# Optimization experiments

Hardware: AMD Instinct MI355X
Metric: run time of the kernel (lower is better)

Reference implementation:

```python
import jax, jax.numpy as jnp
import numpy as np
import math

B, S, DIM, H = 2, 2048, 1024, 16
DH = DIM // H          # 64, per-head dim
DFF = 2048             # FCLayer hidden
NEG = -1.0e9


def setup_inputs() -> dict:
    key = jax.random.key(0)
    ks = jax.random.split(key, 10)
    glorot = jax.nn.initializers.glorot_uniform()
    de_x = jax.random.normal(ks[0], (B, S, DIM), dtype=jnp.float32)
    en_x = jax.random.normal(ks[1], (B, S, DIM), dtype=jnp.float32)
    # causal mask: 1.0 where attention is disallowed (upper triangle)
    mask = jnp.triu(jnp.ones((S, S), dtype=jnp.float32), k=1)
    # Stacked per-head projection weights for the (shared) attn_heads.
    Wq = glorot(ks[2], (H, DIM, DH), jnp.float32)
    Wk = glorot(ks[3], (H, DIM, DH), jnp.float32)
    Wv = glorot(ks[4], (H, DIM, DH), jnp.float32)
    W1 = glorot(ks[5], (DIM, DFF), jnp.float32)
    b1 = jnp.zeros((DFF,), jnp.float32)
    W2 = glorot(ks[6], (DFF, DIM), jnp.float32)
    b2 = jnp.zeros((DIM,), jnp.float32)
    return {"de_x": de_x, "en_x": en_x, "mask": mask,
            "Wq": Wq, "Wk": Wk, "Wv": Wv,
            "W1": W1, "b1": b1, "W2": W2, "b2": b2}


def _multihead(q_x, k_x, v_x, Wq, Wk, Wv, mask):
    # q_x/k_x/v_x: [B,S,DIM]; W*: [H,DIM,DH]
    q = jnp.einsum('bsd,hde->bhse', q_x, Wq)
    k = jnp.einsum('bsd,hde->bhse', k_x, Wk)
    v = jnp.einsum('bsd,hde->bhse', v_x, Wv)
    p = jnp.einsum('bhse,bhte->bhst', q, k) / math.sqrt(DH)
    if mask is not None:
        p = p + mask * NEG
    p = jax.nn.softmax(p, axis=-1)
    h = jnp.einsum('bhst,bhte->bhse', p, v)      # [B,H,S,DH]
    # concat heads along feature dim -> [B,S,DIM]
    return h.transpose(0, 2, 1, 3).reshape(q_x.shape[0], q_x.shape[1], -1)


def reference(de_x, en_x, mask, Wq, Wk, Wv, W1, b1, W2, b2):
    # Faithful to the source: compute_multihead_output ignores its attn_heads
    # arg and always uses self.attn_heads, and binds head(q=outer_en, k=outer_en,
    # v=outer_de). So:
    #   h1 = MHA(q=de_x, k=de_x, v=de_x, mask) with attn_heads weights
    #   h2 = MHA(q=en_x, k=en_x, v=h1, None)   with the SAME weights
    h1 = _multihead(de_x, de_x, de_x, Wq, Wk, Wv, mask)
    h2 = _multihead(en_x, en_x, h1, Wq, Wk, Wv, None)
    ff1 = jax.nn.relu(h2 @ W1 + b1)
    y = ff1 @ W2 + b2
    return y
```

## Files before the change

kernel.cpp:

```cpp
#include <hip/hip_runtime.h>
#include <stdint.h>


#define DEV static __device__ __forceinline__

typedef __attribute__((ext_vector_type(8))) __bf16 bf16x8;
typedef __attribute__((ext_vector_type(8))) unsigned short u16x8;
typedef __attribute__((ext_vector_type(2))) uint32_t u32x2;
typedef __attribute__((ext_vector_type(4))) float f32x4;

DEV float bf2f(uint16_t u) { union { uint32_t u; float f; } v; v.u = ((uint32_t)u) << 16; return v.f; }
DEV uint16_t f2bf(float f) {
  union { float f; uint32_t u; } v; v.f = f;
  uint32_t r = v.u + 0x7fffu + ((v.u >> 16) & 1u);
  return (uint16_t)(r >> 16);
}
DEV uint16_t f2bf_hw(float f) { return __builtin_bit_cast(unsigned short, (__bf16)f); }

DEV bf16x8 asbf(u16x8 v) { return __builtin_bit_cast(bf16x8, v); }
DEV f32x4 mfma32(bf16x8 a, bf16x8 b, f32x4 c) {
  return __builtin_amdgcn_mfma_f32_16x16x32_bf16(a, b, c, 0, 0, 0);
}

DEV void gload_lds16(const void* g, void* l) {
  __builtin_amdgcn_global_load_lds(
      (const __attribute__((address_space(1))) uint32_t*)g,
      (__attribute__((address_space(3))) uint32_t*)l, 16, 0, 0);
}

DEV int swz(int row, int slot) { return slot ^ (row & 7); }

DEV bf16x8 frag8(const uint16_t* l, int row, int slot) {
  u16x8 v = *(const u16x8*)((const char*)l + row * 128 + (swz(row, slot) << 4));
  return asbf(v);
}

__global__ void probe_k(const uint32_t* __restrict__ mask, uint32_t* __restrict__ flag) {
  flag[0] = (mask[1] & 0xFFFFu) ? 1u : 0u;
}

__global__ __launch_bounds__(256) void cvt_k(const void* __restrict__ src,
                                             uint16_t* __restrict__ dst, int n,
                                             const uint32_t* __restrict__ flag) {
  if (flag[0]) return;
  const int stride = gridDim.x * 256 * 8;
  for (int i = (blockIdx.x * 256 + threadIdx.x) * 8; i < n; i += stride) {
    const float* sf = (const float*)src + i;
    u16x8 o;
    for (int j = 0; j < 8; j++) o[j] = f2bf(sf[j]);
    *(u16x8*)(dst + i) = o;
  }
}

__global__ __launch_bounds__(256) void transpose_k(const void* __restrict__ in_,
                                                   uint16_t* __restrict__ out, int R, int C,
                                                   float scale,
                                                   const uint32_t* __restrict__ flag) {
  __shared__ uint16_t t[32][33];
  const int isbf = (int)flag[0];
  const int b = blockIdx.z;
  const float* in_f = (const float*)in_ + (size_t)b * R * C;
  const uint16_t* in_u = (const uint16_t*)in_ + (size_t)b * R * C;
  out += (size_t)b * R * C;
  const int c0 = blockIdx.x * 32, r0 = blockIdx.y * 32;
  const int tx = threadIdx.x & 31, ty = threadIdx.x >> 5;
  for (int i = 0; i < 4; i++) {
    int r = ty + i * 8;
    size_t idx = (size_t)(r0 + r) * C + c0 + tx;
    uint16_t v;
    if (isbf) v = (scale == 1.0f) ? in_u[idx] : f2bf(bf2f(in_u[idx]) * scale);
    else      v = f2bf(in_f[idx] * scale);
    t[r][tx] = v;
  }
  __syncthreads();
  for (int i = 0; i < 4; i++) {
    int r = ty + i * 8;
    out[(size_t)(c0 + r) * R + r0 + tx] = t[tx][r];
  }
}

__global__ __launch_bounds__(256) void transpose_qkv_k(const void* __restrict__ Wq,
                                                       const void* __restrict__ Wk,
                                                       const void* __restrict__ Wv,
                                                       uint16_t* __restrict__ out,
                                                       const uint32_t* __restrict__ flag) {
  __shared__ uint16_t t[32][33];
  const int isbf = (int)flag[0];
  const int which = blockIdx.z >> 4, hh = blockIdx.z & 15;
  const void* in_ = (which == 0 ? Wq : which == 1 ? Wk : Wv);
  const float scale = (which == 0) ? 0.180336880f : 1.0f;
  const int R = 1024, C = 64;
  const float* in_f = (const float*)in_ + (size_t)hh * R * C;
  const uint16_t* in_u = (const uint16_t*)in_ + (size_t)hh * R * C;
  out += ((size_t)which * 16 + hh) * R * C;
  const int c0 = blockIdx.x * 32, r0 = blockIdx.y * 32;
  const int tx = threadIdx.x & 31, ty = threadIdx.x >> 5;
  for (int i = 0; i < 4; i++) {
    int r = ty + i * 8;
    size_t idx = (size_t)(r0 + r) * C + c0 + tx;
    uint16_t v;
    if (isbf) v = (scale == 1.0f) ? in_u[idx] : f2bf(bf2f(in_u[idx]) * scale);
    else      v = f2bf(in_f[idx] * scale);
    t[r][tx] = v;
  }
  __syncthreads();
  for (int i = 0; i < 4; i++) {
    int r = ty + i * 8;
    out[(size_t)(c0 + r) * R + r0 + tx] = t[tx][r];
  }
}

__global__ __launch_bounds__(256) void proj_k(
    const uint16_t* __restrict__ Aqk_c, const void* __restrict__ Aqk_r,
    const uint16_t* __restrict__ Av_c, const void* __restrict__ Av_r,
    const uint16_t* __restrict__ Wt,
    uint16_t* __restrict__ Q, uint16_t* __restrict__ K, uint16_t* __restrict__ Vt,
    const uint32_t* __restrict__ flag) {
  __shared__ __attribute__((aligned(16))) uint16_t lA[2][128 * 64];
  __shared__ __attribute__((aligned(16))) uint16_t lB[2][128 * 64];
  const int isbf = (int)flag[0];
  const uint16_t* Aqk = isbf ? (const uint16_t*)Aqk_r : Aqk_c;
  const uint16_t* Av  = isbf ? (const uint16_t*)Av_r  : Av_c;
  const int tid = threadIdx.x, lane = tid & 63, wave = tid >> 6;
  const int g = lane >> 4;
  const int m0 = blockIdx.x * 128, n0 = blockIdx.y * 128;
  const int proj = n0 >> 10;
  const uint16_t* A = (proj == 2 ? Av : Aqk);
  const uint16_t* Bt = Wt + (size_t)n0 * 1024;
  const int wm = wave >> 1, wn = wave & 1;
  f32x4 acc[4][4] = {};
  u16x8 ra[4], rb[4];
  const int row0 = tid >> 3, slot0 = tid & 7;
  auto loadT = [&](int kt) {
    for (int i = 0; i < 4; i++) {
      int row = row0 + i * 32;
      ra[i] = *(const u16x8*)(A + (size_t)(m0 + row) * 1024 + kt + slot0 * 8);
      rb[i] = *(const u16x8*)(Bt + (size_t)row * 1024 + kt + slot0 * 8);
    }
  };
  auto writeT = [&](int buf) {
    for (int i = 0; i < 4; i++) {
      int row = row0 + i * 32;
      *(u16x8*)&lA[buf][(row * 8 + swz(row, slot0)) * 8] = ra[i];
      *(u16x8*)&lB[buf][(row * 8 + swz(row, slot0)) * 8] = rb[i];
    }
  };
  loadT(0);
  writeT(0);
  int cur = 0;
  for (int it = 0; it < 16; it++) {
    const int more = (it < 15);
    if (more) loadT((it + 1) * 64);
    __syncthreads();
    for (int kk = 0; kk < 2; kk++) {
      bf16x8 af[4], bfr[4];
      for (int fm = 0; fm < 4; fm++) af[fm] = frag8(lA[cur], wm * 64 + fm * 16 + (lane & 15), kk * 4 + g);
      for (int fn = 0; fn < 4; fn++) bfr[fn] = frag8(lB[cur], wn * 64 + fn * 16 + (lane & 15), kk * 4 + g);
      for (int fm = 0; fm < 4; fm++)
        for (int fn = 0; fn < 4; fn++)
          acc[fm][fn] = mfma32(af[fm], bfr[fn], acc[fm][fn]);
    }
    if (more) writeT(cur ^ 1);
    cur ^= 1;
  }
  if (proj != 2) {
    uint16_t* outp = (proj == 0 ? Q : K);
    for (int fm = 0; fm < 4; fm++)
      for (int fn = 0; fn < 4; fn++)
        for (int r = 0; r < 4; r++) {
          int row = m0 + wm * 64 + fm * 16 + g * 4 + r;
          int b = row >> 11, s = row & 2047;
          int col = n0 + wn * 64 + fn * 16 + (lane & 15);
          int h = (col >> 6) & 15, e = col & 63;
          outp[(((size_t)(b * 16 + h)) * 2048 + s) * 64 + e] = f2bf(acc[fm][fn][r]);
        }
  } else {
    __syncthreads();
    uint16_t* tv = (uint16_t*)lA;
    for (int fm = 0; fm < 4; fm++)
      for (int fn = 0; fn < 4; fn++)
        for (int r = 0; r < 4; r++) {
          int rl = wm * 64 + fm * 16 + g * 4 + r;
          int cl = wn * 64 + fn * 16 + (lane & 15);
          int byte = rl * 2;
          *(uint16_t*)((char*)tv + cl * 256 + ((((byte >> 4)) ^ (cl & 15)) << 4) + (byte & 15)) =
              f2bf(acc[fm][fn][r]);
        }
    __syncthreads();
    const int b = m0 >> 11, s0 = m0 & 2047;
    const int c = tid >> 1, half = tid & 1;
    const int col = n0 + c;
    const int h = (col >> 6) & 15, e = col & 63;
    uint16_t* dst = Vt + (((size_t)(b * 16 + h)) * 64 + e) * 2048 + s0 + half * 64;
    for (int j = 0; j < 8; j++) {
      int rl = half * 64 + j * 8;
      u16x8 v = *(const u16x8*)((const char*)tv + c * 256 + (((rl >> 3) ^ (c & 15)) << 4));
      *(u16x8*)(dst + j * 8) = v;
    }
  }
}

__global__ __launch_bounds__(256) void attn1_k(const uint16_t* __restrict__ Q,
                                               const uint16_t* __restrict__ K,
                                               const uint16_t* __restrict__ Vt,
                                               uint16_t* __restrict__ Op0,
                                               uint16_t* __restrict__ Op1,
                                               float* __restrict__ lbuf) {
  __shared__ __attribute__((aligned(16))) uint16_t lK[2][64 * 64];
  __shared__ __attribute__((aligned(16))) uint16_t lV[2][64 * 64];
  __shared__ __attribute__((aligned(16))) uint16_t lP[4][16 * 64];
  const int tid = threadIdx.x, lane = tid & 63, wave = tid >> 6;
  const int g = lane >> 4;
  const int bx = blockIdx.x, h = blockIdx.y, b = blockIdx.z;
  int qt, split, kt0, kt1;
  if (bx < 32) {
    qt = 31 - (bx >> 1);
    split = bx & 1;
    int n0 = (qt + 1) >> 1;
    kt0 = split ? n0 : 0;
    kt1 = split ? (qt + 1) : n0;
  } else {
    qt = 47 - bx; split = 0; kt0 = 0; kt1 = qt + 1;
  }
  const size_t bh = (size_t)(b * 16 + h);
  const uint16_t* Qg = Q + bh * 2048 * 64;
  const uint16_t* Kg = K + bh * 2048 * 64;
  const uint16_t* Vg = Vt + bh * 64 * 2048;
  uint16_t* lPw = lP[wave];
  bf16x8 ones;
  for (int j = 0; j < 8; j++) ones[j] = (__bf16)1.0f;
  const int lrow = lane >> 3, sl = lane & 7;
  auto STAGE = [&](int buf, int kt) {
    for (int i = 0; i < 2; i++) {
      int cb = (i * 4 + wave) * 64;
      int row = (cb >> 3) + lrow;
      int so = swz(row, sl) << 3;
      gload_lds16(Kg + (size_t)(kt * 64 + row) * 64 + so, &lK[buf][cb * 8]);
      gload_lds16(Vg + (size_t)row * 2048 + kt * 64 + so, &lV[buf][cb * 8]);
    }
  };
  const int q0 = qt * 64;
  bf16x8 qf[2];
  {
    int row = q0 + wave * 16 + (lane & 15);
    for (int kk = 0; kk < 2; kk++)
      qf[kk] = asbf(*(const u16x8*)(Qg + (size_t)row * 64 + kk * 32 + g * 8));
  }
  f32x4 oacc[4] = {};
  f32x4 acc_l = {};
  const int qrow = lane & 15;
  STAGE(0, kt0);
  int buf = 0;
  for (int kt = kt0; kt < kt1; kt++) {
    __syncthreads();
    if (kt + 1 < kt1) STAGE(buf ^ 1, kt + 1);
    f32x4 s[4] = {};
    for (int kk = 0; kk < 2; kk++)
      for (int nf = 0; nf < 4; nf++)
        s[nf] = mfma32(frag8(lK[buf], nf * 16 + qrow, kk * 4 + g), qf[kk], s[nf]);
    if (kt == qt) {
      for (int nf = 0; nf < 4; nf++)
        for (int r = 0; r < 4; r++) {
          int kloc = nf * 16 + g * 4 + r;
          if (kloc > wave * 16 + qrow) s[nf][r] = -1e9f;
        }
    }
    for (int nf = 0; nf < 4; nf++) {
      float p0 = __builtin_amdgcn_exp2f(s[nf][0]);
      float p1 = __builtin_amdgcn_exp2f(s[nf][1]);
      float p2 = __builtin_amdgcn_exp2f(s[nf][2]);
      float p3 = __builtin_amdgcn_exp2f(s[nf][3]);
      u32x2 w;
      w[0] = ((uint32_t)f2bf_hw(p1) << 16) | f2bf_hw(p0);
      w[1] = ((uint32_t)f2bf_hw(p3) << 16) | f2bf_hw(p2);
      int slot = 2 * nf + (g >> 1);
      *(u32x2*)((char*)lPw + qrow * 128 + ((slot ^ (qrow & 7)) << 4) + ((g & 1) << 3)) = w;
    }
    for (int kk = 0; kk < 2; kk++) {
      bf16x8 pa = frag8(lPw, qrow, kk * 4 + g);
      acc_l = mfma32(pa, ones, acc_l);
      for (int df = 0; df < 4; df++)
        oacc[df] = mfma32(pa, frag8(lV[buf], df * 16 + qrow, kk * 4 + g), oacc[df]);
    }
    buf ^= 1;
  }
  uint16_t* Op = split ? Op1 : Op0;
  for (int df = 0; df < 4; df++)
    for (int r = 0; r < 4; r++) {
      int srow = q0 + wave * 16 + g * 4 + r;
      int e = df * 16 + qrow;
      Op[((size_t)b * 2048 + srow) * 1024 + h * 64 + e] = f2bf(oacc[df][r]);
    }
  if (qrow == 0) {
    for (int r = 0; r < 4; r++) {
      int srow = q0 + wave * 16 + g * 4 + r;
      lbuf[((size_t)(split * 2 + b) * 16 + h) * 2048 + srow] = acc_l[r];
    }
  }
}

__global__ __launch_bounds__(256) void merge1_k(const uint16_t* __restrict__ O0,
                                                const uint16_t* __restrict__ O1,
                                                const float* __restrict__ lbuf,
                                                uint16_t* __restrict__ out) {
  int i = (blockIdx.x * 256 + threadIdx.x) * 8;
  int sg = i >> 10;
  int b = sg >> 11, s = sg & 2047;
  int h = (i & 1023) >> 6;
  size_t i0 = ((size_t)b * 16 + h) * 2048 + s;
  size_t i1 = ((size_t)(2 + b) * 16 + h) * 2048 + s;
  float l0 = lbuf[i0];
  u16x8 o0 = *(const u16x8*)(O0 + i);
  bool two = (s >> 6) >= 16;
  u16x8 o;
  if (two) {
    float inv = 1.f / (l0 + lbuf[i1]);
    u16x8 o1v = *(const u16x8*)(O1 + i);
    for (int j = 0; j < 8; j++)
      o[j] = f2bf((bf2f(o0[j]) + bf2f(o1v[j])) * inv);
  } else {
    float inv = 1.f / l0;
    for (int j = 0; j < 8; j++) o[j] = f2bf(bf2f(o0[j]) * inv);
  }
  *(u16x8*)(out + i) = o;
}

__global__ __launch_bounds__(256) void attn2_k(const uint16_t* __restrict__ Q,
                                               const uint16_t* __restrict__ K,
                                               const uint16_t* __restrict__ Vt,
                                               uint16_t* __restrict__ Op0,
                                               uint16_t* __restrict__ Op1,
                                               uint16_t* __restrict__ Op2,
                                               uint16_t* __restrict__ Op3,
                                               float* __restrict__ lbuf) {
  __shared__ __attribute__((aligned(16))) uint16_t lK[2][64 * 64];
  __shared__ __attribute__((aligned(16))) uint16_t lV[2][64 * 64];
  __shared__ __attribute__((aligned(16))) uint16_t lP[8][16 * 64];
  const int tid = threadIdx.x, lane = tid & 63, wave = tid >> 6;
  const int g = lane >> 4, qrow = lane & 15;
  const int bx = blockIdx.x, h = blockIdx.y, b = blockIdx.z;
  const int pair = bx >> 2, split = bx & 3;
  const int kt0 = split * 8, kt1 = kt0 + 8;
  const int q0 = pair * 128;
  const size_t bh = (size_t)(b * 16 + h);
  const uint16_t* Qg = Q + bh * 2048 * 64;
  const uint16_t* Kg = K + bh * 2048 * 64;
  const uint16_t* Vg = Vt + bh * 64 * 2048;
  uint16_t* lP0 = lP[wave * 2];
  uint16_t* lP1 = lP[wave * 2 + 1];
  bf16x8 ones;
  for (int j = 0; j < 8; j++) ones[j] = (__bf16)1.0f;
  const int lrow = lane >> 3, sl = lane & 7;
  auto STAGE = [&](int buf, int kt) {
    for (int i = 0; i < 2; i++) {
      int cb = (i * 4 + wave) * 64;
      int row = (cb >> 3) + lrow;
      int so = swz(row, sl) << 3;
      gload_lds16(Kg + (size_t)(kt * 64 + row) * 64 + so, &lK[buf][cb * 8]);
      gload_lds16(Vg + (size_t)row * 2048 + kt * 64 + so, &lV[buf][cb * 8]);
    }
  };
  bf16x8 qf[2][2];
#pragma unroll
  for (int grp = 0; grp < 2; grp++) {
    int row = q0 + grp * 64 + wave * 16 + qrow;
    for (int kk = 0; kk < 2; kk++)
      qf[grp][kk] = asbf(*(const u16x8*)(Qg + (size_t)row * 64 + kk * 32 + g * 8));
  }
  f32x4 oacc[2][4] = {};
  f32x4 acc_l[2] = {};
  auto storeP = [&](uint16_t* lPw, f32x4 (&s)[4]) {
#pragma unroll
    for (int nf = 0; nf < 4; nf++) {
      float p0 = __builtin_amdgcn_exp2f(s[nf][0]);
      float p1 = __builtin_amdgcn_exp2f(s[nf][1]);
      float p2 = __builtin_amdgcn_exp2f(s[nf][2]);
      float p3 = __builtin_amdgcn_exp2f(s[nf][3]);
      u32x2 w;
      w[0] = ((uint32_t)f2bf_hw(p1) << 16) | f2bf_hw(p0);
      w[1] = ((uint32_t)f2bf_hw(p3) << 16) | f2bf_hw(p2);
      int slot = 2 * nf + (g >> 1);
      *(u32x2*)((char*)lPw + qrow * 128 + ((slot ^ (qrow & 7)) << 4) + ((g & 1) << 3)) = w;
    }
  };
  STAGE(0, kt0);
  int buf = 0;
  for (int kt = kt0; kt < kt1; kt++) {
    __syncthreads();
    if (kt + 1 < kt1) STAGE(buf ^ 1, kt + 1);
    f32x4 s0[4] = {}, s1[4] = {};
#pragma unroll
    for (int kk = 0; kk < 2; kk++)
#pragma unroll
      for (int nf = 0; nf < 4; nf++) {
        bf16x8 kf = frag8(lK[buf], nf * 16 + qrow, kk * 4 + g);
        s0[nf] = mfma32(kf, qf[0][kk], s0[nf]);
        s1[nf] = mfma32(kf, qf[1][kk], s1[nf]);
      }
    storeP(lP0, s0);
    storeP(lP1, s1);
#pragma unroll
    for (int kk = 0; kk < 2; kk++) {
      bf16x8 pa0 = frag8(lP0, qrow, kk * 4 + g);
      bf16x8 pa1 = frag8(lP1, qrow, kk * 4 + g);
      acc_l[0] = mfma32(pa0, ones, acc_l[0]);
      acc_l[1] = mfma32(pa1, ones, acc_l[1]);
#pragma unroll
      for (int df = 0; df < 4; df++) {
        bf16x8 vf = frag8(lV[buf], df * 16 + qrow, kk * 4 + g);
        oacc[0][df] = mfma32(pa0, vf, oacc[0][df]);
        oacc[1][df] = mfma32(pa1, vf, oacc[1][df]);
      }
    }
    buf ^= 1;
  }
  uint16_t* Op = (split == 0) ? Op0 : (split == 1) ? Op1 : (split == 2) ? Op2 : Op3;
#pragma unroll
  for (int grp = 0; grp < 2; grp++)
    for (int df = 0; df < 4; df++)
      for (int r = 0; r < 4; r++) {
        int srow = q0 + grp * 64 + wave * 16 + g * 4 + r;
        int e = df * 16 + qrow;
        Op[((size_t)b * 2048 + srow) * 1024 + h * 64 + e] = f2bf(oacc[grp][df][r]);
      }
  if (qrow == 0) {
#pragma unroll
    for (int grp = 0; grp < 2; grp++)
      for (int r = 0; r < 4; r++) {
        int srow = q0 + grp * 64 + wave * 16 + g * 4 + r;
        lbuf[((size_t)(split * 2 + b) * 16 + h) * 2048 + srow] = acc_l[grp][r];
      }
  }
}

__global__ __launch_bounds__(256) void merge2_k(const uint16_t* __restrict__ O0,
                                                const uint16_t* __restrict__ O1,
                                                const uint16_t* __restrict__ O2,
                                                const uint16_t* __restrict__ O3,
                                                const float* __restrict__ lbuf,
                                                uint16_t* __restrict__ out) {
  int i = (blockIdx.x * 256 + threadIdx.x) * 8;
  int sg = i >> 10;
  int b = sg >> 11, s = sg & 2047;
  int h = (i & 1023) >> 6;
  float l = 0.f;
  for (int sp = 0; sp < 4; sp++)
    l += lbuf[((size_t)(sp * 2 + b) * 16 + h) * 2048 + s];
  float inv = 1.f / l;
  u16x8 o0 = *(const u16x8*)(O0 + i);
  u16x8 o1 = *(const u16x8*)(O1 + i);
  u16x8 o2 = *(const u16x8*)(O2 + i);
  u16x8 o3 = *(const u16x8*)(O3 + i);
  u16x8 o;
  for (int j = 0; j < 8; j++)
    o[j] = f2bf((bf2f(o0[j]) + bf2f(o1[j]) + bf2f(o2[j]) + bf2f(o3[j])) * inv);
  *(u16x8*)(out + i) = o;
}

template <int RELU>
__global__ __launch_bounds__(256) void ff_k(const uint16_t* __restrict__ A,
                                            const uint16_t* __restrict__ Bt,
                                            const void* __restrict__ bias,
                                            uint16_t* __restrict__ C, int Kdim, int N,
                                            const uint32_t* __restrict__ flag) {
  __shared__ __attribute__((aligned(16))) uint16_t lA[2][128 * 64];
  __shared__ __attribute__((aligned(16))) uint16_t lB[2][128 * 64];
  const int isbf = (int)flag[0];
  const int tid = threadIdx.x, lane = tid & 63, wave = tid >> 6;
  const int g = lane >> 4;
  const int m0 = blockIdx.x * 128, n0 = blockIdx.y * 128;
  const int wm = wave >> 1, wn = wave & 1;
  f32x4 acc[4][4] = {};
  u16x8 ra[4], rb[4];
  const int row0 = tid >> 3, slot0 = tid & 7;
  auto loadT = [&](int kt) {
    for (int i = 0; i < 4; i++) {
      int row = row0 + i * 32;
      ra[i] = *(const u16x8*)(A + (size_t)(m0 + row) * Kdim + kt + slot0 * 8);
      rb[i] = *(const u16x8*)(Bt + (size_t)(n0 + row) * Kdim + kt + slot0 * 8);
    }
  };
  auto writeT = [&](int buf) {
    for (int i = 0; i < 4; i++) {
      int row = row0 + i * 32;
      *(u16x8*)&lA[buf][(row * 8 + swz(row, slot0)) * 8] = ra[i];
      *(u16x8*)&lB[buf][(row * 8 + swz(row, slot0)) * 8] = rb[i];
    }
  };
  loadT(0);
  writeT(0);
  int cur = 0;
  const int nit = Kdim >> 6;
  for (int it = 0; it < nit; it++) {
    const int more = (it < nit - 1);
    if (more) loadT((it + 1) * 64);
    __syncthreads();
    for (int kk = 0; kk < 2; kk++) {
      bf16x8 af[4], bfr[4];
      for (int fm = 0; fm < 4; fm++) af[fm] = frag8(lA[cur], wm * 64 + fm * 16 + (lane & 15), kk * 4 + g);
      for (int fn = 0; fn < 4; fn++) bfr[fn] = frag8(lB[cur], wn * 64 + fn * 16 + (lane & 15), kk * 4 + g);
      for (int fm = 0; fm < 4; fm++)
        for (int fn = 0; fn < 4; fn++)
          acc[fm][fn] = mfma32(af[fm], bfr[fn], acc[fm][fn]);
    }
    if (more) writeT(cur ^ 1);
    cur ^= 1;
  }
  for (int fm = 0; fm < 4; fm++)
    for (int fn = 0; fn < 4; fn++) {
      int col = n0 + wn * 64 + fn * 16 + (lane & 15);
      float bv = isbf ? bf2f(((const uint16_t*)bias)[col]) : ((const float*)bias)[col];
      for (int r = 0; r < 4; r++) {
        int row = m0 + wm * 64 + fm * 16 + g * 4 + r;
        float v = acc[fm][fn][r] + bv;
        if (RELU) v = fmaxf(v, 0.f);
        C[(size_t)row * N + col] = f2bf(v);
      }
    }
}

__global__ __launch_bounds__(256) void store_k(const uint16_t* __restrict__ yb,
                                               void* __restrict__ out, int n,
                                               const uint32_t* __restrict__ flag) {
  const int isbf = (int)flag[0];
  const int stride = gridDim.x * 256 * 8;
  for (int i = (blockIdx.x * 256 + threadIdx.x) * 8; i < n; i += stride) {
    u16x8 v = *(const u16x8*)(yb + i);
    if (isbf) {
      *(u16x8*)((uint16_t*)out + i) = v;
    } else {
      float* of = (float*)out + i;
      for (int j = 0; j < 8; j++) of[j] = bf2f(v[j]);
    }
  }
}

extern "C" void kernel_launch(void* const* d_in, const int* in_sizes, int n_in,
                              void* d_out, int out_size, void* d_ws, size_t ws_size,
                              hipStream_t stream) {
  const void* de_x = d_in[0];
  const void* en_x = d_in[1];
  const void* mask = d_in[2];
  const void* Wq = d_in[3];
  const void* Wk = d_in[4];
  const void* Wv = d_in[5];
  const void* W1 = d_in[6];
  const void* b1 = d_in[7];
  const void* W2 = d_in[8];
  const void* b2 = d_in[9];

  uint16_t* ws = (uint16_t*)d_ws;
  const size_t M1 = (size_t)1 << 20;
  uint32_t* flag = (uint32_t*)ws;
  float* lbuf = (float*)(ws + 8192);
  uint16_t* Wtq = ws + 1 * M1;
  uint16_t* W1t = ws + 4 * M1;
  uint16_t* W2t = ws + 6 * M1;
  uint16_t* de_c = ws + 8 * M1;
  uint16_t* en_c = ws + 12 * M1;
  uint16_t* Qb  = ws + 16 * M1;
  uint16_t* Kb  = ws + 20 * M1;
  uint16_t* Vtb = ws + 24 * M1;
  uint16_t* h1  = ws + 28 * M1;
  uint16_t* h2  = ws + 32 * M1;
  uint16_t* ff1 = Qb;
  uint16_t* yb  = Vtb;

  const int NX = 2 * 2048 * 1024;
  dim3 blk(256);

  probe_k<<<1, 1, 0, stream>>>((const uint32_t*)mask, flag);
  cvt_k<<<2048, blk, 0, stream>>>(de_x, de_c, NX, flag);
  cvt_k<<<2048, blk, 0, stream>>>(en_x, en_c, NX, flag);
  transpose_qkv_k<<<dim3(2, 32, 48), blk, 0, stream>>>(Wq, Wk, Wv, Wtq, flag);
  transpose_k<<<dim3(64, 32, 1), blk, 0, stream>>>(W1, W1t, 1024, 2048, 1.0f, flag);
  transpose_k<<<dim3(32, 64, 1), blk, 0, stream>>>(W2, W2t, 2048, 1024, 1.0f, flag);
  proj_k<<<dim3(32, 24), blk, 0, stream>>>(de_c, de_x, de_c, de_x, Wtq, Qb, Kb, Vtb, flag);
  attn1_k<<<dim3(48, 16, 2), blk, 0, stream>>>(Qb, Kb, Vtb, de_c, h2, lbuf);
  merge1_k<<<2048, blk, 0, stream>>>(de_c, h2, lbuf, h1);
  proj_k<<<dim3(32, 24), blk, 0, stream>>>(en_c, en_x, h1, h1, Wtq, Qb, Kb, Vtb, flag);
  attn2_k<<<dim3(64, 16, 2), blk, 0, stream>>>(Qb, Kb, Vtb, de_c, en_c, h1, h2, lbuf);
  merge2_k<<<2048, blk, 0, stream>>>(de_c, en_c, h1, h2, lbuf, h2);
  ff_k<1><<<dim3(32, 16), blk, 0, stream>>>(h2, W1t, b1, ff1, 1024, 2048, flag);
  ff_k<0><<<dim3(32, 8), blk, 0, stream>>>(ff1, W2t, b2, yb, 2048, 1024, flag);
  store_k<<<2048, blk, 0, stream>>>(yb, d_out, out_size, flag);
}
```

Before: 270.5 us.

## Unify causal and full attention into templated kernel with two-tile K/V reuse

Replaces the causal single-tile attention kernel with a templated attention kernel in which each block handles two 64-row query tiles and shares every staged K/V tile between them. The causal case splits the key range into three chunks of 12 tiles, skips the first query tile's MFMAs on tiles past its diagonal, and masks diagonal tiles. A three-way merge kernel replaces the old two-way merge. This is meant to halve K/V staging traffic per query row. In exchange, blocks whose key chunk is empty, or is only partly useful for one of the two query tiles, add idle or imbalanced work, and the merge now always reads three partial buffers.

```diff
diff --git a/kernel.cpp b/kernel.cpp
--- a/kernel.cpp
+++ b/kernel.cpp
@@ -200,148 +200,33 @@
   }
 }
 
-__global__ __launch_bounds__(256) void attn1_k(const uint16_t* __restrict__ Q,
-                                               const uint16_t* __restrict__ K,
-                                               const uint16_t* __restrict__ Vt,
-                                               uint16_t* __restrict__ Op0,
-                                               uint16_t* __restrict__ Op1,
-                                               float* __restrict__ lbuf) {
-  __shared__ __attribute__((aligned(16))) uint16_t lK[2][64 * 64];
-  __shared__ __attribute__((aligned(16))) uint16_t lV[2][64 * 64];
-  __shared__ __attribute__((aligned(16))) uint16_t lP[4][16 * 64];
-  const int tid = threadIdx.x, lane = tid & 63, wave = tid >> 6;
-  const int g = lane >> 4;
-  const int bx = blockIdx.x, h = blockIdx.y, b = blockIdx.z;
-  int qt, split, kt0, kt1;
-  if (bx < 32) {
-    qt = 31 - (bx >> 1);
-    split = bx & 1;
-    int n0 = (qt + 1) >> 1;
-    kt0 = split ? n0 : 0;
-    kt1 = split ? (qt + 1) : n0;
-  } else {
-    qt = 47 - bx; split = 0; kt0 = 0; kt1 = qt + 1;
-  }
-  const size_t bh = (size_t)(b * 16 + h);
-  const uint16_t* Qg = Q + bh * 2048 * 64;
-  const uint16_t* Kg = K + bh * 2048 * 64;
-  const uint16_t* Vg = Vt + bh * 64 * 2048;
-  uint16_t* lPw = lP[wave];
-  bf16x8 ones;
-  for (int j = 0; j < 8; j++) ones[j] = (__bf16)1.0f;
-  const int lrow = lane >> 3, sl = lane & 7;
-  auto STAGE = [&](int buf, int kt) {
-    for (int i = 0; i < 2; i++) {
-      int cb = (i * 4 + wave) * 64;
-      int row = (cb >> 3) + lrow;
-      int so = swz(row, sl) << 3;
-      gload_lds16(Kg + (size_t)(kt * 64 + row) * 64 + so, &lK[buf][cb * 8]);
-      gload_lds16(Vg + (size_t)row * 2048 + kt * 64 + so, &lV[buf][cb * 8]);
-    }
-  };
-  const int q0 = qt * 64;
-  bf16x8 qf[2];
-  {
-    int row = q0 + wave * 16 + (lane & 15);
-    for (int kk = 0; kk < 2; kk++)
-      qf[kk] = asbf(*(const u16x8*)(Qg + (size_t)row * 64 + kk * 32 + g * 8));
-  }
-  f32x4 oacc[4] = {};
-  f32x4 acc_l = {};
-  const int qrow = lane & 15;
-  STAGE(0, kt0);
-  int buf = 0;
-  for (int kt = kt0; kt < kt1; kt++) {
-    __syncthreads();
-    if (kt + 1 < kt1) STAGE(buf ^ 1, kt + 1);
-    f32x4 s[4] = {};
-    for (int kk = 0; kk < 2; kk++)
-      for (int nf = 0; nf < 4; nf++)
-        s[nf] = mfma32(frag8(lK[buf], nf * 16 + qrow, kk * 4 + g), qf[kk], s[nf]);
-    if (kt == qt) {
-      for (int nf = 0; nf < 4; nf++)
-        for (int r = 0; r < 4; r++) {
-          int kloc = nf * 16 + g * 4 + r;
-          if (kloc > wave * 16 + qrow) s[nf][r] = -1e9f;
-        }
-    }
-    for (int nf = 0; nf < 4; nf++) {
-      float p0 = __builtin_amdgcn_exp2f(s[nf][0]);
-      float p1 = __builtin_amdgcn_exp2f(s[nf][1]);
-      float p2 = __builtin_amdgcn_exp2f(s[nf][2]);
-      float p3 = __builtin_amdgcn_exp2f(s[nf][3]);
-      u32x2 w;
-      w[0] = ((uint32_t)f2bf_hw(p1) << 16) | f2bf_hw(p0);
-      w[1] = ((uint32_t)f2bf_hw(p3) << 16) | f2bf_hw(p2);
-      int slot = 2 * nf + (g >> 1);
-      *(u32x2*)((char*)lPw + qrow * 128 + ((slot ^ (qrow & 7)) << 4) + ((g & 1) << 3)) = w;
-    }
-    for (int kk = 0; kk < 2; kk++) {
-      bf16x8 pa = frag8(lPw, qrow, kk * 4 + g);
-      acc_l = mfma32(pa, ones, acc_l);
-      for (int df = 0; df < 4; df++)
-        oacc[df] = mfma32(pa, frag8(lV[buf], df * 16 + qrow, kk * 4 + g), oacc[df]);
-    }
-    buf ^= 1;
-  }
-  uint16_t* Op = split ? Op1 : Op0;
-  for (int df = 0; df < 4; df++)
-    for (int r = 0; r < 4; r++) {
-      int srow = q0 + wave * 16 + g * 4 + r;
-      int e = df * 16 + qrow;
-      Op[((size_t)b * 2048 + srow) * 1024 + h * 64 + e] = f2bf(oacc[df][r]);
-    }
-  if (qrow == 0) {
-    for (int r = 0; r < 4; r++) {
-      int srow = q0 + wave * 16 + g * 4 + r;
-      lbuf[((size_t)(split * 2 + b) * 16 + h) * 2048 + srow] = acc_l[r];
-    }
-  }
-}
-
-__global__ __launch_bounds__(256) void merge1_k(const uint16_t* __restrict__ O0,
-                                                const uint16_t* __restrict__ O1,
-                                                const float* __restrict__ lbuf,
-                                                uint16_t* __restrict__ out) {
-  int i = (blockIdx.x * 256 + threadIdx.x) * 8;
-  int sg = i >> 10;
-  int b = sg >> 11, s = sg & 2047;
-  int h = (i & 1023) >> 6;
-  size_t i0 = ((size_t)b * 16 + h) * 2048 + s;
-  size_t i1 = ((size_t)(2 + b) * 16 + h) * 2048 + s;
-  float l0 = lbuf[i0];
-  u16x8 o0 = *(const u16x8*)(O0 + i);
-  bool two = (s >> 6) >= 16;
-  u16x8 o;
-  if (two) {
-    float inv = 1.f / (l0 + lbuf[i1]);
-    u16x8 o1v = *(const u16x8*)(O1 + i);
-    for (int j = 0; j < 8; j++)
-      o[j] = f2bf((bf2f(o0[j]) + bf2f(o1v[j])) * inv);
-  } else {
-    float inv = 1.f / l0;
-    for (int j = 0; j < 8; j++) o[j] = f2bf(bf2f(o0[j]) * inv);
-  }
-  *(u16x8*)(out + i) = o;
-}
-
-__global__ __launch_bounds__(256) void attn2_k(const uint16_t* __restrict__ Q,
-                                               const uint16_t* __restrict__ K,
-                                               const uint16_t* __restrict__ Vt,
-                                               uint16_t* __restrict__ Op0,
-                                               uint16_t* __restrict__ Op1,
-                                               uint16_t* __restrict__ Op2,
-                                               uint16_t* __restrict__ Op3,
-                                               float* __restrict__ lbuf) {
+template <int CAUSAL>
+__global__ __launch_bounds__(256) void attn_k(const uint16_t* __restrict__ Q,
+                                              const uint16_t* __restrict__ K,
+                                              const uint16_t* __restrict__ Vt,
+                                              uint16_t* __restrict__ Op0,
+                                              uint16_t* __restrict__ Op1,
+                                              uint16_t* __restrict__ Op2,
+                                              uint16_t* __restrict__ Op3,
+                                              float* __restrict__ lbuf) {
   __shared__ __attribute__((aligned(16))) uint16_t lK[2][64 * 64];
   __shared__ __attribute__((aligned(16))) uint16_t lV[2][64 * 64];
   __shared__ __attribute__((aligned(16))) uint16_t lP[8][16 * 64];
   const int tid = threadIdx.x, lane = tid & 63, wave = tid >> 6;
   const int g = lane >> 4, qrow = lane & 15;
   const int bx = blockIdx.x, h = blockIdx.y, b = blockIdx.z;
-  const int pair = bx >> 2, split = bx & 3;
-  const int kt0 = split * 8, kt1 = kt0 + 8;
+  int pair, split, kt0, kt1;
+  if (CAUSAL) {
+    pair = 15 - bx / 3;
+    split = bx - (bx / 3) * 3;
+    kt0 = split * 12;
+    int lim = 2 * pair + 2;
+    kt1 = (kt0 + 12 < lim) ? kt0 + 12 : lim;
+  } else {
+    pair = bx >> 2; split = bx & 3; kt0 = split * 8; kt1 = kt0 + 8;
+  }
   const int q0 = pair * 128;
+  const int qt0 = pair * 2, qt1 = pair * 2 + 1;
   const size_t bh = (size_t)(b * 16 + h);
   const uint16_t* Qg = Q + bh * 2048 * 64;
   const uint16_t* Kg = K + bh * 2048 * 64;
@@ -360,13 +245,6 @@
       gload_lds16(Vg + (size_t)row * 2048 + kt * 64 + so, &lV[buf][cb * 8]);
     }
   };
-  bf16x8 qf[2][2];
-#pragma unroll
-  for (int grp = 0; grp < 2; grp++) {
-    int row = q0 + grp * 64 + wave * 16 + qrow;
-    for (int kk = 0; kk < 2; kk++)
-      qf[grp][kk] = asbf(*(const u16x8*)(Qg + (size_t)row * 64 + kk * 32 + g * 8));
-  }
   f32x4 oacc[2][4] = {};
   f32x4 acc_l[2] = {};
   auto storeP = [&](uint16_t* lPw, f32x4 (&s)[4]) {
@@ -383,36 +261,61 @@
       *(u32x2*)((char*)lPw + qrow * 128 + ((slot ^ (qrow & 7)) << 4) + ((g & 1) << 3)) = w;
     }
   };
-  STAGE(0, kt0);
-  int buf = 0;
-  for (int kt = kt0; kt < kt1; kt++) {
-    __syncthreads();
-    if (kt + 1 < kt1) STAGE(buf ^ 1, kt + 1);
-    f32x4 s0[4] = {}, s1[4] = {};
-#pragma unroll
-    for (int kk = 0; kk < 2; kk++)
-#pragma unroll
-      for (int nf = 0; nf < 4; nf++) {
-        bf16x8 kf = frag8(lK[buf], nf * 16 + qrow, kk * 4 + g);
-        s0[nf] = mfma32(kf, qf[0][kk], s0[nf]);
-        s1[nf] = mfma32(kf, qf[1][kk], s1[nf]);
+  if (kt0 < kt1) {
+    bf16x8 qf[2][2];
+#pragma unroll
+    for (int grp = 0; grp < 2; grp++) {
+      int row = q0 + grp * 64 + wave * 16 + qrow;
+      for (int kk = 0; kk < 2; kk++)
+        qf[grp][kk] = asbf(*(const u16x8*)(Qg + (size_t)row * 64 + kk * 32 + g * 8));
+    }
+    STAGE(0, kt0);
+    int buf = 0;
+    for (int kt = kt0; kt < kt1; kt++) {
+      __syncthreads();
+      if (kt + 1 < kt1) STAGE(buf ^ 1, kt + 1);
+      const bool c0 = !CAUSAL || (kt <= qt0);
+      f32x4 s0[4] = {}, s1[4] = {};
+#pragma unroll
+      for (int kk = 0; kk < 2; kk++)
+#pragma unroll
+        for (int nf = 0; nf < 4; nf++) {
+          bf16x8 kf = frag8(lK[buf], nf * 16 + qrow, kk * 4 + g);
+          if (c0) s0[nf] = mfma32(kf, qf[0][kk], s0[nf]);
+          s1[nf] = mfma32(kf, qf[1][kk], s1[nf]);
+        }
+      if (CAUSAL && kt == qt0) {
+#pragma unroll
+        for (int nf = 0; nf < 4; nf++)
+          for (int r = 0; r < 4; r++)
+            if (nf * 16 + g * 4 + r > wave * 16 + qrow) s0[nf][r] = -1e9f;
       }
-    storeP(lP0, s0);
-    storeP(lP1, s1);
-#pragma unroll
-    for (int kk = 0; kk < 2; kk++) {
-      bf16x8 pa0 = frag8(lP0, qrow, kk * 4 + g);
-      bf16x8 pa1 = frag8(lP1, qrow, kk * 4 + g);
-      acc_l[0] = mfma32(pa0, ones, acc_l[0]);
-      acc_l[1] = mfma32(pa1, ones, acc_l[1]);
-#pragma unroll
-      for (int df = 0; df < 4; df++) {
-        bf16x8 vf = frag8(lV[buf], df * 16 + qrow, kk * 4 + g);
-        oacc[0][df] = mfma32(pa0, vf, oacc[0][df]);
-        oacc[1][df] = mfma32(pa1, vf, oacc[1][df]);
+      if (CAUSAL && kt == qt1) {
+#pragma unroll
+        for (int nf = 0; nf < 4; nf++)
+          for (int r = 0; r < 4; r++)
+            if (nf * 16 + g * 4 + r > wave * 16 + qrow) s1[nf][r] = -1e9f;
       }
-    }
-    buf ^= 1;
+      if (c0) storeP(lP0, s0);
+      storeP(lP1, s1);
+#pragma unroll
+      for (int kk = 0; kk < 2; kk++) {
+        bf16x8 pa0, pa1;
+        if (c0) {
+          pa0 = frag8(lP0, qrow, kk * 4 + g);
+          acc_l[0] = mfma32(pa0, ones, acc_l[0]);
+        }
+        pa1 = frag8(lP1, qrow, kk * 4 + g);
+        acc_l[1] = mfma32(pa1, ones, acc_l[1]);
+#pragma unroll
+        for (int df = 0; df < 4; df++) {
+          bf16x8 vf = frag8(lV[buf], df * 16 + qrow, kk * 4 + g);
+          if (c0) oacc[0][df] = mfma32(pa0, vf, oacc[0][df]);
+          oacc[1][df] = mfma32(pa1, vf, oacc[1][df]);
+        }
+      }
+      buf ^= 1;
+    }
   }
   uint16_t* Op = (split == 0) ? Op0 : (split == 1) ? Op1 : (split == 2) ? Op2 : Op3;
 #pragma unroll
@@ -433,7 +336,29 @@
   }
 }
 
-__global__ __launch_bounds__(256) void merge2_k(const uint16_t* __restrict__ O0,
+__global__ __launch_bounds__(256) void merge3_k(const uint16_t* __restrict__ O0,
+                                                const uint16_t* __restrict__ O1,
+                                                const uint16_t* __restrict__ O2,
+                                                const float* __restrict__ lbuf,
+                                                uint16_t* __restrict__ out) {
+  int i = (blockIdx.x * 256 + threadIdx.x) * 8;
+  int sg = i >> 10;
+  int b = sg >> 11, s = sg & 2047;
+  int h = (i & 1023) >> 6;
+  float l = 0.f;
+  for (int sp = 0; sp < 3; sp++)
+    l += lbuf[((size_t)(sp * 2 + b) * 16 + h) * 2048 + s];
+  float inv = 1.f / l;
+  u16x8 o0 = *(const u16x8*)(O0 + i);
+  u16x8 o1 = *(const u16x8*)(O1 + i);
+  u16x8 o2 = *(const u16x8*)(O2 + i);
+  u16x8 o;
+  for (int j = 0; j < 8; j++)
+    o[j] = f2bf((bf2f(o0[j]) + bf2f(o1[j]) + bf2f(o2[j])) * inv);
+  *(u16x8*)(out + i) = o;
+}
+
+__global__ __launch_bounds__(256) void merge4_k(const uint16_t* __restrict__ O0,
                                                 const uint16_t* __restrict__ O1,
                                                 const uint16_t* __restrict__ O2,
                                                 const uint16_t* __restrict__ O3,
@@ -576,11 +501,11 @@
   transpose_k<<<dim3(64, 32, 1), blk, 0, stream>>>(W1, W1t, 1024, 2048, 1.0f, flag);
   transpose_k<<<dim3(32, 64, 1), blk, 0, stream>>>(W2, W2t, 2048, 1024, 1.0f, flag);
   proj_k<<<dim3(32, 24), blk, 0, stream>>>(de_c, de_x, de_c, de_x, Wtq, Qb, Kb, Vtb, flag);
-  attn1_k<<<dim3(48, 16, 2), blk, 0, stream>>>(Qb, Kb, Vtb, de_c, h2, lbuf);
-  merge1_k<<<2048, blk, 0, stream>>>(de_c, h2, lbuf, h1);
+  attn_k<1><<<dim3(48, 16, 2), blk, 0, stream>>>(Qb, Kb, Vtb, de_c, h2, h1, h1, lbuf);
+  merge3_k<<<2048, blk, 0, stream>>>(de_c, h2, h1, lbuf, h1);
   proj_k<<<dim3(32, 24), blk, 0, stream>>>(en_c, en_x, h1, h1, Wtq, Qb, Kb, Vtb, flag);
-  attn2_k<<<dim3(64, 16, 2), blk, 0, stream>>>(Qb, Kb, Vtb, de_c, en_c, h1, h2, lbuf);
-  merge2_k<<<2048, blk, 0, stream>>>(de_c, en_c, h1, h2, lbuf, h2);
+  attn_k<0><<<dim3(64, 16, 2), blk, 0, stream>>>(Qb, Kb, Vtb, de_c, en_c, h1, h2, lbuf);
+  merge4_k<<<2048, blk, 0, stream>>>(de_c, en_c, h1, h2, lbuf, h2);
   ff_k<1><<<dim3(32, 16), blk, 0, stream>>>(h2, W1t, b1, ff1, 1024, 2048, flag);
   ff_k<0><<<dim3(32, 8), blk, 0, stream>>>(ff1, W2t, b2, yb, 2048, 1024, flag);
   store_k<<<2048, blk, 0, stream>>>(yb, d_out, out_size, flag);
```

After: 293.8 us. +8.6%, slower.
